# Kernel optimization log

Hardware: AMD Instinct MI355X
Metric: run time of the kernel (lower is better)

## Reference

```python
import jax, jax.numpy as jnp
import numpy as np

R_MAX, S_MAX, TOKEN_Z = 32, 2, 128
N_IN = 4 * (R_MAX + 1) + 2 * (S_MAX + 1) + 1  # 139
B, L = 1, 1024


def setup_inputs() -> dict:
    key = jax.random.key(0)
    k1, k2, k3, k4, k5 = jax.random.split(key, 5)
    asym_id = jnp.sort(jax.random.randint(k1, (B, L), 0, 8), axis=-1)
    residue_index = jnp.sort(jax.random.randint(k2, (B, L), 0, 512), axis=-1)
    entity_id = jax.random.randint(k3, (B, L), 0, 4)
    token_index = jnp.arange(B * L, dtype=jnp.int64 if jax.config.jax_enable_x64 else jnp.int32).reshape(B, L)
    sym_id = jax.random.randint(k4, (B, L), 0, 4)
    cyclic_period = jnp.zeros((B, L), dtype=jnp.int32)
    W = jax.random.normal(k5, (N_IN, TOKEN_Z), dtype=jnp.float32) * 0.02
    return {
        "asym_id": asym_id,
        "residue_index": residue_index,
        "entity_id": entity_id,
        "token_index": token_index,
        "sym_id": sym_id,
        "cyclic_period": cyclic_period,
        "W": W,
    }


def reference(asym_id, residue_index, entity_id, token_index, sym_id, cyclic_period, W):
    # Pairwise boolean masks [B, L, L]
    same_chain = asym_id[:, :, None] == asym_id[:, None, :]
    same_residue = residue_index[:, :, None] == residue_index[:, None, :]
    same_entity = entity_id[:, :, None] == entity_id[:, None, :]

    rel_pos = residue_index[:, :, None] - residue_index[:, None, :]
    # Cyclic wrap: period=10000 where cyclic_period<=0 is a no-op for |rel_pos|<5000
    period = jnp.where(cyclic_period > 0, cyclic_period, 10000)[:, None, :]
    rel_pos = rel_pos - (period * jnp.round(rel_pos / period)).astype(rel_pos.dtype)

    d_residue = jnp.clip(rel_pos + R_MAX, 0, 2 * R_MAX)
    d_residue = jnp.where(same_chain, d_residue, 2 * R_MAX + 1)

    d_token = jnp.clip(token_index[:, :, None] - token_index[:, None, :] + R_MAX, 0, 2 * R_MAX)
    d_token = jnp.where(same_chain & same_residue, d_token, 2 * R_MAX + 1)

    d_chain = jnp.clip(sym_id[:, :, None] - sym_id[:, None, :] + S_MAX, 0, 2 * S_MAX)
    d_chain = jnp.where(same_chain, 2 * S_MAX + 1, d_chain)

    # onehot(d) @ W == gather of W rows: fuse concat+onehot+linear into gathers + sum.
    n_rel = 2 * R_MAX + 2  # 66
    n_ch = 2 * S_MAX + 2   # 6
    W_pos = W[:n_rel]
    W_tok = W[n_rel:2 * n_rel]
    w_ent = W[2 * n_rel]
    W_ch = W[2 * n_rel + 1:2 * n_rel + 1 + n_ch]

    p = (W_pos[d_residue]
         + W_tok[d_token]
         + same_entity[..., None].astype(W.dtype) * w_ent
         + W_ch[d_chain])  # [B, L, L, token_z]
    return p
```

## Files before the change

kernel.cpp:

```cpp
#include <hip/hip_runtime.h>

#define TZ 128
#define JT 256
#define IT 8
#define R_MAX 32
#define S_MAX 2
#define NROW 139

typedef float v4f __attribute__((ext_vector_type(4)));

__global__ __launch_bounds__(256, 2) void relpos_kernel(
    const int* __restrict__ asym, const int* __restrict__ resi,
    const int* __restrict__ ent,  const int* __restrict__ tok,
    const int* __restrict__ sym,  const int* __restrict__ cyc,
    const float* __restrict__ W,  float* __restrict__ out, int L)
{
    __shared__ v4f sW[NROW * 32];
    __shared__ unsigned int sidx[IT * JT];

    const int i0  = blockIdx.x * IT;
    const int j0  = blockIdx.y * JT;
    const int tid = threadIdx.x;

    const v4f* __restrict__ Wv = (const v4f*)W;

    for (int idx = tid; idx < NROW * 32; idx += 256)
        sW[idx] = Wv[idx];

    {
        const int j  = j0 + tid;
        const int aj = asym[j], rj = resi[j], ej = ent[j];
        const int tj = tok[j],  sj = sym[j],  cj = cyc[j];
        const int period = (cj > 0) ? cj : 10000;
        const float inv_p = 1.0f / (float)period;

        #pragma unroll
        for (int ii = 0; ii < IT; ++ii) {
            const int i  = i0 + ii;
            const int ai = asym[i], ri = resi[i], ei = ent[i];
            const int ti = tok[i],  si = sym[i];

            const bool same_chain = (ai == aj);
            const bool same_res   = (ri == rj);
            const bool same_ent   = (ei == ej);

            int rel = ri - rj;
            const float q = rintf((float)rel * inv_p);
            rel -= (int)((float)period * q);

            int dr = rel + R_MAX;
            dr = dr < 0 ? 0 : (dr > 2 * R_MAX ? 2 * R_MAX : dr);
            if (!same_chain) dr = 2 * R_MAX + 1;

            int dt = ti - tj + R_MAX;
            dt = dt < 0 ? 0 : (dt > 2 * R_MAX ? 2 * R_MAX : dt);
            if (!(same_chain && same_res)) dt = 2 * R_MAX + 1;

            int dc = si - sj + S_MAX;
            dc = dc < 0 ? 0 : (dc > 2 * S_MAX ? 2 * S_MAX : dc);
            if (same_chain) dc = 2 * S_MAX + 1;

            sidx[ii * JT + tid] = (unsigned)dr | ((unsigned)dt << 8)
                                | ((unsigned)dc << 16)
                                | ((unsigned)(same_ent ? 1u : 0u) << 24);
        }
    }

    const int zq = tid & 31;
    const int jr = tid >> 5;
    const v4f we = Wv[132 * 32 + zq];

    __syncthreads();

    for (int ii = 0; ii < IT; ++ii) {
        v4f* __restrict__ outp =
            (v4f*)(out + ((size_t)(i0 + ii) * (size_t)L + (size_t)j0) * TZ);
        const unsigned* __restrict__ sip = &sidx[ii * JT + jr * 32];

        #pragma unroll 2
        for (int it4 = 0; it4 < 8; ++it4) {
            const uint4 pk4 = *(const uint4*)&sip[it4 * 4];

            #pragma unroll
            for (int k = 0; k < 4; ++k) {
                const unsigned pk = (&pk4.x)[k];
                const int dr = pk & 0xFF;
                const int dt = (pk >> 8) & 0xFF;
                const int dc = (pk >> 16) & 0xFF;
                const float se = (pk >> 24) ? 1.0f : 0.0f;

                const v4f a = sW[dr * 32 + zq];
                const v4f b = sW[(66 + dt) * 32 + zq];
                const v4f c = sW[(133 + dc) * 32 + zq];

                const int jl = jr * 32 + it4 * 4 + k;
                __builtin_nontemporal_store(a + b + c + se * we,
                                            &outp[jl * 32 + zq]);
            }
        }
    }
}

extern "C" void kernel_launch(void* const* d_in, const int* in_sizes, int n_in,
                              void* d_out, int out_size, void* d_ws, size_t ws_size,
                              hipStream_t stream) {
    const int* asym = (const int*)d_in[0];
    const int* resi = (const int*)d_in[1];
    const int* ent  = (const int*)d_in[2];
    const int* tok  = (const int*)d_in[3];
    const int* sym  = (const int*)d_in[4];
    const int* cyc  = (const int*)d_in[5];
    const float* W  = (const float*)d_in[6];
    float* out      = (float*)d_out;

    const int L = in_sizes[0];
    dim3 grid(L / IT, L / JT);
    dim3 block(256);
    relpos_kernel<<<grid, block, 0, stream>>>(asym, resi, ent, tok, sym, cyc, W, out, L);
}
```

Before: 534.1 us.

## Retile to two full output rows per block with interleaved row stores

```diff
diff --git a/kernel.cpp b/kernel.cpp
--- a/kernel.cpp
+++ b/kernel.cpp
@@ -1,8 +1,6 @@
 #include <hip/hip_runtime.h>
 
 #define TZ 128
-#define JT 256
-#define IT 8
 #define R_MAX 32
 #define S_MAX 2
 #define NROW 139
@@ -16,53 +14,57 @@
     const float* __restrict__ W,  float* __restrict__ out, int L)
 {
     __shared__ v4f sW[NROW * 32];
-    __shared__ unsigned int sidx[IT * JT];
+    __shared__ unsigned int sidx[2 * 1024];
 
-    const int i0  = blockIdx.x * IT;
-    const int j0  = blockIdx.y * JT;
     const int tid = threadIdx.x;
+    const int i0  = blockIdx.x * 2;
 
     const v4f* __restrict__ Wv = (const v4f*)W;
 
     for (int idx = tid; idx < NROW * 32; idx += 256)
         sW[idx] = Wv[idx];
 
-    {
-        const int j  = j0 + tid;
+    int ai_[2], ri_[2], ei_[2], ti_[2], si_[2];
+    #pragma unroll
+    for (int ii = 0; ii < 2; ++ii) {
+        ai_[ii] = asym[i0 + ii]; ri_[ii] = resi[i0 + ii]; ei_[ii] = ent[i0 + ii];
+        ti_[ii] = tok[i0 + ii];  si_[ii] = sym[i0 + ii];
+    }
+
+    #pragma unroll
+    for (int q = 0; q < 4; ++q) {
+        const int j  = q * 256 + tid;
         const int aj = asym[j], rj = resi[j], ej = ent[j];
         const int tj = tok[j],  sj = sym[j],  cj = cyc[j];
         const int period = (cj > 0) ? cj : 10000;
         const float inv_p = 1.0f / (float)period;
+        const int tr = (j & 7) * 128 + (j >> 3);
 
         #pragma unroll
-        for (int ii = 0; ii < IT; ++ii) {
-            const int i  = i0 + ii;
-            const int ai = asym[i], ri = resi[i], ei = ent[i];
-            const int ti = tok[i],  si = sym[i];
+        for (int ii = 0; ii < 2; ++ii) {
+            const bool same_chain = (ai_[ii] == aj);
+            const bool same_res   = (ri_[ii] == rj);
+            const bool same_ent   = (ei_[ii] == ej);
 
-            const bool same_chain = (ai == aj);
-            const bool same_res   = (ri == rj);
-            const bool same_ent   = (ei == ej);
-
-            int rel = ri - rj;
-            const float q = rintf((float)rel * inv_p);
-            rel -= (int)((float)period * q);
+            int rel = ri_[ii] - rj;
+            const float qq = rintf((float)rel * inv_p);
+            rel -= (int)((float)period * qq);
 
             int dr = rel + R_MAX;
             dr = dr < 0 ? 0 : (dr > 2 * R_MAX ? 2 * R_MAX : dr);
             if (!same_chain) dr = 2 * R_MAX + 1;
 
-            int dt = ti - tj + R_MAX;
+            int dt = ti_[ii] - tj + R_MAX;
             dt = dt < 0 ? 0 : (dt > 2 * R_MAX ? 2 * R_MAX : dt);
             if (!(same_chain && same_res)) dt = 2 * R_MAX + 1;
 
-            int dc = si - sj + S_MAX;
+            int dc = si_[ii] - sj + S_MAX;
             dc = dc < 0 ? 0 : (dc > 2 * S_MAX ? 2 * S_MAX : dc);
             if (same_chain) dc = 2 * S_MAX + 1;
 
-            sidx[ii * JT + tid] = (unsigned)dr | ((unsigned)dt << 8)
-                                | ((unsigned)dc << 16)
-                                | ((unsigned)(same_ent ? 1u : 0u) << 24);
+            sidx[ii * 1024 + tr] = (unsigned)dr | ((unsigned)dt << 8)
+                                 | ((unsigned)dc << 16)
+                                 | ((unsigned)(same_ent ? 1u : 0u) << 24);
         }
     }
 
@@ -72,14 +74,16 @@
 
     __syncthreads();
 
-    for (int ii = 0; ii < IT; ++ii) {
-        v4f* __restrict__ outp =
-            (v4f*)(out + ((size_t)(i0 + ii) * (size_t)L + (size_t)j0) * TZ);
-        const unsigned* __restrict__ sip = &sidx[ii * JT + jr * 32];
+    v4f* __restrict__ outv = (v4f*)out + (size_t)blockIdx.x * (2 * 1024 * 32);
+
+    #pragma unroll
+    for (int ii = 0; ii < 2; ++ii) {
+        const unsigned* __restrict__ sip = &sidx[ii * 1024 + jr * 128];
+        v4f* __restrict__ op = outv + ii * 32768 + zq;
 
         #pragma unroll 2
-        for (int it4 = 0; it4 < 8; ++it4) {
-            const uint4 pk4 = *(const uint4*)&sip[it4 * 4];
+        for (int t4 = 0; t4 < 32; ++t4) {
+            const uint4 pk4 = *(const uint4*)&sip[t4 * 4];
 
             #pragma unroll
             for (int k = 0; k < 4; ++k) {
@@ -93,9 +97,8 @@
                 const v4f b = sW[(66 + dt) * 32 + zq];
                 const v4f c = sW[(133 + dc) * 32 + zq];
 
-                const int jl = jr * 32 + it4 * 4 + k;
-                __builtin_nontemporal_store(a + b + c + se * we,
-                                            &outp[jl * 32 + zq]);
+                const int t = t4 * 4 + k;
+                op[(t * 8 + jr) * 32] = a + b + c + se * we;
             }
         }
     }
@@ -114,7 +117,7 @@
     float* out      = (float*)d_out;
 
     const int L = in_sizes[0];
-    dim3 grid(L / IT, L / JT);
+    dim3 grid(L / 2);
     dim3 block(256);
     relpos_kernel<<<grid, block, 0, stream>>>(asym, resi, ent, tok, sym, cyc, W, out, L);
 }
```

Measured after the change: 537.0 us. Within noise of the previous version (+0.6%).
